# Performance work log

Hardware: AMD Instinct MI355X
Metric: run time of the kernel (lower is better)

Reference implementation:

```python
import jax, jax.numpy as jnp
import numpy as np

B, LH, HF = 65536, 128, 32
VC_MIN = 0.0


def _theta_init():
    # Deterministic parameter init, matching the torch constructor defaults.
    def spinv(x):
        return float(np.log(np.exp(max(x, 1e-4)) - 1.0 + 1e-6))
    vals = [
        0.0,                                  # alpha_raw: log(0.5/(1-0.5))
        float(np.log(np.exp(1.0) - 1.0 + 1e-6)),   # c_raw  (c_init=1.0)
        float(np.log(np.exp(0.1) - 1.0 + 1e-6)),   # kappa_raw (kappa_init=0.1)
        float(np.log(np.exp(0.15) - 1.0 + 1e-6)),  # vc_raw (vc_eff=0.15)
        -6.0,   # log_qx
        -6.0,   # log_qu
        -5.0,   # log_r
        0.0,    # log_q_scale
        -6.0,   # log_p0_xx
        -4.0,   # log_p0_uu
        spinv(0.1),   # a1_raw
        spinv(0.05),  # d1_raw
        spinv(0.5),   # d2_raw
        spinv(0.5),   # d3_raw
        0.0,    # b1
        0.0,    # b2
        0.1,    # beta
        float(np.arctanh(0.9)),  # rho_m_raw
        -4.0,   # log_qm
        -4.0,   # log_p0_mm
    ]
    return np.asarray(vals, dtype=np.float32)


def setup_inputs() -> dict:
    key = jax.random.key(0)
    k1, k2, k3, k4, k5 = jax.random.split(key, 5)
    return {
        "v_hist": jax.random.normal(k1, (B, LH), dtype=jnp.float32),
        "dt_hist": 0.01 + 0.1 * jax.random.uniform(k2, (B, LH), dtype=jnp.float32),
        "x_obs_hist": jax.random.normal(k3, (B, LH), dtype=jnp.float32),
        "v_fut": jax.random.normal(k4, (B, HF), dtype=jnp.float32),
        "dt_fut": 0.01 + 0.1 * jax.random.uniform(k5, (B, HF), dtype=jnp.float32),
        "theta": jnp.asarray(_theta_init()),
    }


def _forward(v_hist, dt_hist, x_obs_hist, v_fut, dt_fut, theta):
    sp = jax.nn.softplus
    alpha = jax.nn.sigmoid(theta[0])
    c = sp(theta[1]); kappa = sp(theta[2]); vc = sp(theta[3]) + VC_MIN
    qx = jnp.exp(theta[4]); qu = jnp.exp(theta[5]); R = jnp.exp(theta[6])
    qs = jnp.exp(theta[7]); p0xx = jnp.exp(theta[8]); p0uu = jnp.exp(theta[9])
    a1 = sp(theta[10]); d1 = sp(theta[11]); d2 = sp(theta[12]); d3 = sp(theta[13])
    b1 = theta[14]; b2 = theta[15]; beta = theta[16]
    rho_m = jnp.tanh(theta[17]); qm = jnp.exp(theta[18]); p0mm = jnp.exp(theta[19])

    Bn, Lh = v_hist.shape
    dtype = v_hist.dtype
    eye = jnp.eye(3, dtype=dtype)

    def predict(s, P, v, dv, dt):
        x, u, m = s[:, 0], s[:, 1], s[:, 2]
        rho = jnp.exp(-alpha * dt)
        forcing = jax.nn.relu(v * v - vc * vc)
        cl = (-a1 * u + b1 * v + b2 * dv
              - d1 * u * u - d2 * u * jnp.abs(v) - d3 * u * jnp.abs(u))
        x_p = x + u * dt
        u_p = rho * u - kappa * x * dt + c * forcing * dt + cl * dt + beta * m
        m_p = rho_m * m
        s_p = jnp.stack([x_p, u_p, m_p], axis=1)
        z = jnp.zeros_like(dt); o = jnp.ones_like(dt)
        Fm = jnp.stack([
            jnp.stack([o, dt, z], axis=1),
            jnp.stack([-kappa * dt, rho, beta * o], axis=1),
            jnp.stack([z, z, rho_m * o], axis=1)], axis=1)  # [B,3,3]
        qdiag = jnp.stack([qs * qx * dt, qs * qu * dt, qm * o], axis=1)  # [B,3]
        P_p = jnp.einsum('bij,bjk,blk->bil', Fm, P, Fm) + qdiag[:, :, None] * eye
        return s_p, P_p

    def update(s, P, y):
        innov = y - s[:, 0]
        S = P[:, 0, 0] + R
        K = P[:, :, 0] / S[:, None]            # [B,3]
        s_u = s + K * innov[:, None]
        IKH = eye - K[:, :, None] * eye[0]     # I - K H, H = [1,0,0]
        P_u = (jnp.einsum('bij,bjk,blk->bil', IKH, P, IKH)
               + R * (K[:, :, None] * K[:, None, :]))
        return s_u, P_u

    s0 = jnp.zeros((Bn, 3), dtype).at[:, 0].set(x_obs_hist[:, 0])
    P0 = jnp.broadcast_to(jnp.diag(jnp.stack([p0xx, p0uu, p0mm])).astype(dtype),
                          (Bn, 3, 3))

    # History steps k = 1 .. Lh-1 (scan over time axis, [T, B] layout)
    v_h = v_hist[:, :Lh - 1].T
    dv_h = jnp.concatenate(
        [jnp.zeros((1, Bn), dtype), (v_hist[:, 1:Lh - 1] - v_hist[:, :Lh - 2]).T], axis=0)
    dt_h = jnp.maximum(dt_hist[:, 1:], 1e-6).T
    y_h = x_obs_hist[:, 1:].T

    def hist_step(carry, inp):
        s, P = carry
        v, dv, dt, y = inp
        s, P = predict(s, P, v, dv, dt)
        s, P = update(s, P, y)
        return (s, P), None

    (s, P), _ = jax.lax.scan(hist_step, (s0, P0), (v_h, dv_h, dt_h, y_h))

    # Future rollout (predict only)
    v_f = v_fut.T
    dv_f = (v_fut - jnp.concatenate([v_hist[:, -1:], v_fut[:, :-1]], axis=1)).T
    dt_f = jnp.maximum(dt_fut, 1e-6).T

    def fut_step(carry, inp):
        s, P = carry
        v, dv, dt = inp
        s, P = predict(s, P, v, dv, dt)
        return (s, P), (s[:, 0], P[:, 0, 0], s[:, 1])

    _, (x_preds, x_vars, u_ests) = jax.lax.scan(fut_step, (s, P), (v_f, dv_f, dt_f))
    return x_preds.T, x_vars.T, u_ests.T  # each [B, Hf]


def reference(v_hist, dt_hist, x_obs_hist, v_fut, dt_fut, theta):
    return _forward(v_hist, dt_hist, x_obs_hist, v_fut, dt_fut, theta)
```

## Files before the change

kernel.cpp:

```cpp
#include <hip/hip_runtime.h>
#include <math.h>

#define BATCH 65536
#define LHIST 128
#define HFUT  32

__device__ __forceinline__ float softplusf(float x) {
    return fmaxf(x, 0.0f) + log1pf(expf(-fabsf(x)));
}

__global__ __launch_bounds__(256) void kalman_fwd(
    const float* __restrict__ v_hist,
    const float* __restrict__ dt_hist,
    const float* __restrict__ x_obs,
    const float* __restrict__ v_fut,
    const float* __restrict__ dt_fut,
    const float* __restrict__ theta,
    float* __restrict__ out)
{
    const int b = blockIdx.x * blockDim.x + threadIdx.x;

    const float alpha = 1.0f / (1.0f + expf(-theta[0]));
    const float c     = softplusf(theta[1]);
    const float kappa = softplusf(theta[2]);
    const float vc    = softplusf(theta[3]);
    const float qx    = expf(theta[4]);
    const float qu    = expf(theta[5]);
    const float Rn    = expf(theta[6]);
    const float qs    = expf(theta[7]);
    const float p0xx  = expf(theta[8]);
    const float p0uu  = expf(theta[9]);
    const float a1    = softplusf(theta[10]);
    const float d1    = softplusf(theta[11]);
    const float d2    = softplusf(theta[12]);
    const float d3    = softplusf(theta[13]);
    const float b1    = theta[14];
    const float b2    = theta[15];
    const float beta  = theta[16];
    const float rho_m = tanhf(theta[17]);
    const float qm    = expf(theta[18]);
    const float p0mm  = expf(theta[19]);
    const float vc2   = vc * vc;
    const float qxs   = qs * qx;
    const float qus   = qs * qu;

    float sx, su = 0.0f, sm = 0.0f;
    float p00 = p0xx, p01 = 0.0f, p02 = 0.0f, p11 = p0uu, p12 = 0.0f, p22 = p0mm;

    auto predict = [&](float v, float dv, float dt_raw) {
        float dt  = fmaxf(dt_raw, 1e-6f);
        float rho = expf(-alpha * dt);
        float forcing = fmaxf(v * v - vc2, 0.0f);
        float cl = -a1 * su + b1 * v + b2 * dv
                 - d1 * su * su - d2 * su * fabsf(v) - d3 * su * fabsf(su);
        float kdt = kappa * dt;
        float x_p = sx + su * dt;
        float u_p = rho * su - kdt * sx + c * forcing * dt + cl * dt + beta * sm;
        float m_p = rho_m * sm;
        float f0 = p00 + dt * p01;
        float f1 = p01 + dt * p11;
        float f2 = p02 + dt * p12;
        float g0 = -kdt * p00 + rho * p01 + beta * p02;
        float g1 = -kdt * p01 + rho * p11 + beta * p12;
        float g2 = -kdt * p02 + rho * p12 + beta * p22;
        float n00 = f0 + dt * f1 + qxs * dt;
        float n01 = -kdt * f0 + rho * f1 + beta * f2;
        float n02 = rho_m * f2;
        float n11 = -kdt * g0 + rho * g1 + beta * g2 + qus * dt;
        float n12 = rho_m * g2;
        float n22 = rho_m * rho_m * p22 + qm;
        sx = x_p; su = u_p; sm = m_p;
        p00 = n00; p01 = n01; p02 = n02; p11 = n11; p12 = n12; p22 = n22;
    };

    auto update = [&](float y) {
        float innov = y - sx;
        float S    = p00 + Rn;
        float Sinv = __builtin_amdgcn_rcpf(S);
        float K0 = p00 * Sinv, K1 = p01 * Sinv, K2 = p02 * Sinv;
        sx += K0 * innov; su += K1 * innov; sm += K2 * innov;
        float a = 1.0f - K0;
        float n00 = a * a * p00 + Rn * K0 * K0;
        float n01 = a * (p01 - K1 * p00) + Rn * K0 * K1;
        float n02 = a * (p02 - K2 * p00) + Rn * K0 * K2;
        float n11 = S * K1 * K1 - 2.0f * K1 * p01 + p11;
        float n12 = S * K1 * K2 - K2 * p01 - K1 * p02 + p12;
        float n22 = S * K2 * K2 - 2.0f * K2 * p02 + p22;
        p00 = n00; p01 = n01; p02 = n02; p11 = n11; p12 = n12; p22 = n22;
    };

    const float4* v4 = (const float4*)(v_hist  + (size_t)b * LHIST);
    const float4* d4 = (const float4*)(dt_hist + (size_t)b * LHIST);
    const float4* y4 = (const float4*)(x_obs   + (size_t)b * LHIST);

    float4 vq = v4[0], dq = d4[0], yq = y4[0];
    float4 vn = v4[1], dn = d4[1], yn = y4[1];
    sx = yq.x;

    predict(vq.x, 0.0f,        dq.y); update(yq.y);
    predict(vq.y, vq.y - vq.x, dq.z); update(yq.z);
    predict(vq.z, vq.z - vq.y, dq.w); update(yq.w);

    #pragma unroll 1
    for (int q = 1; q < 31; ++q) {
        float4 v2 = v4[q + 1], d2 = d4[q + 1], y2 = y4[q + 1];
        predict(vq.w, vq.w - vq.z, dn.x); update(yn.x);
        predict(vn.x, vn.x - vq.w, dn.y); update(yn.y);
        predict(vn.y, vn.y - vn.x, dn.z); update(yn.z);
        predict(vn.z, vn.z - vn.y, dn.w); update(yn.w);
        vq = vn; vn = v2; dn = d2; yn = y2;
    }
    predict(vq.w, vq.w - vq.z, dn.x); update(yn.x);
    predict(vn.x, vn.x - vq.w, dn.y); update(yn.y);
    predict(vn.y, vn.y - vn.x, dn.z); update(yn.z);
    predict(vn.z, vn.z - vn.y, dn.w); update(yn.w);
    float v_prev = vn.w;

    const float4* vf4 = (const float4*)(v_fut  + (size_t)b * HFUT);
    const float4* df4 = (const float4*)(dt_fut + (size_t)b * HFUT);
    float4* xp = (float4*)(out + (size_t)b * HFUT);
    float4* xv = (float4*)(out + (size_t)BATCH * HFUT + (size_t)b * HFUT);
    float4* ue = (float4*)(out + 2 * (size_t)BATCH * HFUT + (size_t)b * HFUT);

    #pragma unroll 1
    for (int q = 0; q < HFUT / 4; ++q) {
        float4 vf = vf4[q], df = df4[q];
        float4 oxp, oxv, oue;
        predict(vf.x, vf.x - v_prev, df.x); oxp.x = sx; oxv.x = p00; oue.x = su;
        predict(vf.y, vf.y - vf.x,   df.y); oxp.y = sx; oxv.y = p00; oue.y = su;
        predict(vf.z, vf.z - vf.y,   df.z); oxp.z = sx; oxv.z = p00; oue.z = su;
        predict(vf.w, vf.w - vf.z,   df.w); oxp.w = sx; oxv.w = p00; oue.w = su;
        v_prev = vf.w;
        xp[q] = oxp; xv[q] = oxv; ue[q] = oue;
    }
}

extern "C" void kernel_launch(void* const* d_in, const int* in_sizes, int n_in,
                              void* d_out, int out_size, void* d_ws, size_t ws_size,
                              hipStream_t stream) {
    const float* v_hist  = (const float*)d_in[0];
    const float* dt_hist = (const float*)d_in[1];
    const float* x_obs   = (const float*)d_in[2];
    const float* v_fut   = (const float*)d_in[3];
    const float* dt_fut  = (const float*)d_in[4];
    const float* theta   = (const float*)d_in[5];
    float* out = (float*)d_out;

    dim3 grid(BATCH / 256), block(256);
    hipLaunchKernelGGL(kalman_fwd, grid, block, 0, stream,
                       v_hist, dt_hist, x_obs, v_fut, dt_fut, theta, out);
}
```

Before: 199.0 us.

## Batch history loads in 32-step register chunks and prefetch future inputs

The history loop now loads 32 timesteps of v, dt and y into register arrays per chunk and fully unrolls the filter steps inside each chunk. Previously it prefetched only one float4 ahead. The future inputs are loaded up front, and all future outputs are buffered in registers and written at the end. Launch bounds are set to one block minimum, which allows many more registers. The aim is more memory-level parallelism and fewer load stalls, at the cost of much higher register pressure, lower occupancy and possible spills.

```diff
diff --git a/kernel.cpp b/kernel.cpp
--- a/kernel.cpp
+++ b/kernel.cpp
@@ -9,7 +9,7 @@
     return fmaxf(x, 0.0f) + log1pf(expf(-fabsf(x)));
 }
 
-__global__ __launch_bounds__(256) void kalman_fwd(
+__global__ __launch_bounds__(256, 1) void kalman_fwd(
     const float* __restrict__ v_hist,
     const float* __restrict__ dt_hist,
     const float* __restrict__ x_obs,
@@ -44,7 +44,7 @@
     const float qxs   = qs * qx;
     const float qus   = qs * qu;
 
-    float sx, su = 0.0f, sm = 0.0f;
+    float sx = 0.0f, su = 0.0f, sm = 0.0f;
     float p00 = p0xx, p01 = 0.0f, p02 = 0.0f, p11 = p0uu, p12 = 0.0f, p22 = p0mm;
 
     auto predict = [&](float v, float dv, float dt_raw) {
@@ -89,49 +89,62 @@
         p00 = n00; p01 = n01; p02 = n02; p11 = n11; p12 = n12; p22 = n22;
     };
 
-    const float4* v4 = (const float4*)(v_hist  + (size_t)b * LHIST);
-    const float4* d4 = (const float4*)(dt_hist + (size_t)b * LHIST);
-    const float4* y4 = (const float4*)(x_obs   + (size_t)b * LHIST);
+    const float4* v4  = (const float4*)(v_hist  + (size_t)b * LHIST);
+    const float4* d4  = (const float4*)(dt_hist + (size_t)b * LHIST);
+    const float4* y4  = (const float4*)(x_obs   + (size_t)b * LHIST);
+    const float4* vf4 = (const float4*)(v_fut   + (size_t)b * HFUT);
+    const float4* df4 = (const float4*)(dt_fut  + (size_t)b * HFUT);
 
-    float4 vq = v4[0], dq = d4[0], yq = y4[0];
-    float4 vn = v4[1], dn = d4[1], yn = y4[1];
-    sx = yq.x;
+    float vf[HFUT], df[HFUT];
+    {
+        float4* VF = (float4*)vf; float4* DF = (float4*)df;
+        #pragma unroll
+        for (int i = 0; i < HFUT / 4; ++i) { VF[i] = vf4[i]; DF[i] = df4[i]; }
+    }
 
-    predict(vq.x, 0.0f,        dq.y); update(yq.y);
-    predict(vq.y, vq.y - vq.x, dq.z); update(yq.z);
-    predict(vq.z, vq.z - vq.y, dq.w); update(yq.w);
+    float v_bridge = 0.0f, dv_bridge = 0.0f;
 
     #pragma unroll 1
-    for (int q = 1; q < 31; ++q) {
-        float4 v2 = v4[q + 1], d2 = d4[q + 1], y2 = y4[q + 1];
-        predict(vq.w, vq.w - vq.z, dn.x); update(yn.x);
-        predict(vn.x, vn.x - vq.w, dn.y); update(yn.y);
-        predict(vn.y, vn.y - vn.x, dn.z); update(yn.z);
-        predict(vn.z, vn.z - vn.y, dn.w); update(yn.w);
-        vq = vn; vn = v2; dn = d2; yn = y2;
+    for (int k = 0; k < 4; ++k) {
+        float vv[32], dd[32], yy[32];
+        float4* V = (float4*)vv; float4* D = (float4*)dd; float4* Y = (float4*)yy;
+        #pragma unroll
+        for (int i = 0; i < 8; ++i) {
+            V[i] = v4[8 * k + i];
+            D[i] = d4[8 * k + i];
+            Y[i] = y4[8 * k + i];
+        }
+        if (k == 0) {
+            sx = yy[0];
+            predict(vv[0], 0.0f, dd[1]); update(yy[1]);
+        } else {
+            predict(v_bridge, dv_bridge, dd[0]); update(yy[0]);
+            predict(vv[0], vv[0] - v_bridge, dd[1]); update(yy[1]);
+        }
+        #pragma unroll
+        for (int i = 1; i < 31; ++i) {
+            predict(vv[i], vv[i] - vv[i - 1], dd[i + 1]); update(yy[i + 1]);
+        }
+        v_bridge  = vv[31];
+        dv_bridge = vv[31] - vv[30];
     }
-    predict(vq.w, vq.w - vq.z, dn.x); update(yn.x);
-    predict(vn.x, vn.x - vq.w, dn.y); update(yn.y);
-    predict(vn.y, vn.y - vn.x, dn.z); update(yn.z);
-    predict(vn.z, vn.z - vn.y, dn.w); update(yn.w);
-    float v_prev = vn.w;
 
-    const float4* vf4 = (const float4*)(v_fut  + (size_t)b * HFUT);
-    const float4* df4 = (const float4*)(dt_fut + (size_t)b * HFUT);
+    float oxp[HFUT], oxv[HFUT], oue[HFUT];
+    float vp = v_bridge;
+    #pragma unroll
+    for (int j = 0; j < HFUT; ++j) {
+        predict(vf[j], vf[j] - vp, df[j]);
+        vp = vf[j];
+        oxp[j] = sx; oxv[j] = p00; oue[j] = su;
+    }
+
     float4* xp = (float4*)(out + (size_t)b * HFUT);
     float4* xv = (float4*)(out + (size_t)BATCH * HFUT + (size_t)b * HFUT);
     float4* ue = (float4*)(out + 2 * (size_t)BATCH * HFUT + (size_t)b * HFUT);
-
-    #pragma unroll 1
-    for (int q = 0; q < HFUT / 4; ++q) {
-        float4 vf = vf4[q], df = df4[q];
-        float4 oxp, oxv, oue;
-        predict(vf.x, vf.x - v_prev, df.x); oxp.x = sx; oxv.x = p00; oue.x = su;
-        predict(vf.y, vf.y - vf.x,   df.y); oxp.y = sx; oxv.y = p00; oue.y = su;
-        predict(vf.z, vf.z - vf.y,   df.z); oxp.z = sx; oxv.z = p00; oue.z = su;
-        predict(vf.w, vf.w - vf.z,   df.w); oxp.w = sx; oxv.w = p00; oue.w = su;
-        v_prev = vf.w;
-        xp[q] = oxp; xv[q] = oxv; ue[q] = oue;
+    float4* OXP = (float4*)oxp; float4* OXV = (float4*)oxv; float4* OUE = (float4*)oue;
+    #pragma unroll
+    for (int i = 0; i < HFUT / 4; ++i) {
+        xp[i] = OXP[i]; xv[i] = OXV[i]; ue[i] = OUE[i];
     }
 }
 
```

Result: faster. 186.9 us (-6.1%).

## Double-buffer 16-step history chunks and batch future loads and stores

Applied to the files above, without the earlier changes.

Restructures the history loop into 16-step chunks held in two register buffers (A/B), so each chunk's loads are issued one chunk ahead of its compute. The future rollout now loads all inputs up front, before the last history chunk, and defers every output store to the end. It also swaps expf for a hardware exp2 with a prescaled constant and sets launch bounds to (256,1). The cost being targeted is memory latency per thread. The price is much higher register pressure, which can lower occupancy and reduce latency hiding across waves.

```diff
diff --git a/kernel.cpp b/kernel.cpp
--- a/kernel.cpp
+++ b/kernel.cpp
@@ -9,7 +9,7 @@
     return fmaxf(x, 0.0f) + log1pf(expf(-fabsf(x)));
 }
 
-__global__ __launch_bounds__(256) void kalman_fwd(
+__global__ __launch_bounds__(256, 1) void kalman_fwd(
     const float* __restrict__ v_hist,
     const float* __restrict__ dt_hist,
     const float* __restrict__ x_obs,
@@ -18,7 +18,7 @@
     const float* __restrict__ theta,
     float* __restrict__ out)
 {
-    const int b = blockIdx.x * blockDim.x + threadIdx.x;
+    const int b = blockIdx.x * 256 + threadIdx.x;
 
     const float alpha = 1.0f / (1.0f + expf(-theta[0]));
     const float c     = softplusf(theta[1]);
@@ -43,13 +43,14 @@
     const float vc2   = vc * vc;
     const float qxs   = qs * qx;
     const float qus   = qs * qu;
-
-    float sx, su = 0.0f, sm = 0.0f;
+    const float nal2e = -alpha * 1.44269504088896340736f;
+
+    float sx = 0.0f, su = 0.0f, sm = 0.0f;
     float p00 = p0xx, p01 = 0.0f, p02 = 0.0f, p11 = p0uu, p12 = 0.0f, p22 = p0mm;
 
     auto predict = [&](float v, float dv, float dt_raw) {
         float dt  = fmaxf(dt_raw, 1e-6f);
-        float rho = expf(-alpha * dt);
+        float rho = __builtin_amdgcn_exp2f(nal2e * dt);
         float forcing = fmaxf(v * v - vc2, 0.0f);
         float cl = -a1 * su + b1 * v + b2 * dv
                  - d1 * su * su - d2 * su * fabsf(v) - d3 * su * fabsf(su);
@@ -93,46 +94,100 @@
     const float4* d4 = (const float4*)(dt_hist + (size_t)b * LHIST);
     const float4* y4 = (const float4*)(x_obs   + (size_t)b * LHIST);
 
-    float4 vq = v4[0], dq = d4[0], yq = y4[0];
-    float4 vn = v4[1], dn = d4[1], yn = y4[1];
-    sx = yq.x;
-
-    predict(vq.x, 0.0f,        dq.y); update(yq.y);
-    predict(vq.y, vq.y - vq.x, dq.z); update(yq.z);
-    predict(vq.z, vq.z - vq.y, dq.w); update(yq.w);
+    float4 AV0, AV1, AV2, AV3, AD0, AD1, AD2, AD3, AY0, AY1, AY2, AY3;
+    float4 BV0, BV1, BV2, BV3, BD0, BD1, BD2, BD3, BY0, BY1, BY2, BY3;
+    float vp1 = 0.0f, vp2 = 0.0f;
+
+#define LOAD_CHUNK(k, P) do {                                                    \
+    P##V0 = v4[4*(k)+0]; P##V1 = v4[4*(k)+1];                                    \
+    P##V2 = v4[4*(k)+2]; P##V3 = v4[4*(k)+3];                                    \
+    P##D0 = d4[4*(k)+0]; P##D1 = d4[4*(k)+1];                                    \
+    P##D2 = d4[4*(k)+2]; P##D3 = d4[4*(k)+3];                                    \
+    P##Y0 = y4[4*(k)+0]; P##Y1 = y4[4*(k)+1];                                    \
+    P##Y2 = y4[4*(k)+2]; P##Y3 = y4[4*(k)+3];                                    \
+} while (0)
+
+#define KSTEP(vc_, vpv_, dtn_, yn_) do { predict((vc_), (vc_) - (vpv_), (dtn_)); update(yn_); } while (0)
+
+#define CHUNK_TAIL(P) do {                                                       \
+    KSTEP(P##V0.y, P##V0.x, P##D0.z, P##Y0.z);                                   \
+    KSTEP(P##V0.z, P##V0.y, P##D0.w, P##Y0.w);                                   \
+    KSTEP(P##V0.w, P##V0.z, P##D1.x, P##Y1.x);                                   \
+    KSTEP(P##V1.x, P##V0.w, P##D1.y, P##Y1.y);                                   \
+    KSTEP(P##V1.y, P##V1.x, P##D1.z, P##Y1.z);                                   \
+    KSTEP(P##V1.z, P##V1.y, P##D1.w, P##Y1.w);                                   \
+    KSTEP(P##V1.w, P##V1.z, P##D2.x, P##Y2.x);                                   \
+    KSTEP(P##V2.x, P##V1.w, P##D2.y, P##Y2.y);                                   \
+    KSTEP(P##V2.y, P##V2.x, P##D2.z, P##Y2.z);                                   \
+    KSTEP(P##V2.z, P##V2.y, P##D2.w, P##Y2.w);                                   \
+    KSTEP(P##V2.w, P##V2.z, P##D3.x, P##Y3.x);                                   \
+    KSTEP(P##V3.x, P##V2.w, P##D3.y, P##Y3.y);                                   \
+    KSTEP(P##V3.y, P##V3.x, P##D3.z, P##Y3.z);                                   \
+    KSTEP(P##V3.z, P##V3.y, P##D3.w, P##Y3.w);                                   \
+    vp2 = P##V3.z; vp1 = P##V3.w;                                                \
+} while (0)
+
+#define CHUNK(P) do {                                                            \
+    predict(vp1, vp1 - vp2, P##D0.x);   update(P##Y0.x);                         \
+    KSTEP(P##V0.x, vp1, P##D0.y, P##Y0.y);                                       \
+    CHUNK_TAIL(P);                                                               \
+} while (0)
+
+    LOAD_CHUNK(0, A);
+    LOAD_CHUNK(1, B);
+
+    sx = AY0.x;
+    predict(AV0.x, 0.0f, AD0.y); update(AY0.y);
+    CHUNK_TAIL(A);
 
     #pragma unroll 1
-    for (int q = 1; q < 31; ++q) {
-        float4 v2 = v4[q + 1], d2 = d4[q + 1], y2 = y4[q + 1];
-        predict(vq.w, vq.w - vq.z, dn.x); update(yn.x);
-        predict(vn.x, vn.x - vq.w, dn.y); update(yn.y);
-        predict(vn.y, vn.y - vn.x, dn.z); update(yn.z);
-        predict(vn.z, vn.z - vn.y, dn.w); update(yn.w);
-        vq = vn; vn = v2; dn = d2; yn = y2;
+    for (int k = 1; k <= 3; ++k) {
+        LOAD_CHUNK(2 * k, A);
+        CHUNK(B);
+        LOAD_CHUNK(2 * k + 1, B);
+        CHUNK(A);
     }
-    predict(vq.w, vq.w - vq.z, dn.x); update(yn.x);
-    predict(vn.x, vn.x - vq.w, dn.y); update(yn.y);
-    predict(vn.y, vn.y - vn.x, dn.z); update(yn.z);
-    predict(vn.z, vn.z - vn.y, dn.w); update(yn.w);
-    float v_prev = vn.w;
 
     const float4* vf4 = (const float4*)(v_fut  + (size_t)b * HFUT);
     const float4* df4 = (const float4*)(dt_fut + (size_t)b * HFUT);
+    float4 VF0 = vf4[0], VF1 = vf4[1], VF2 = vf4[2], VF3 = vf4[3],
+           VF4 = vf4[4], VF5 = vf4[5], VF6 = vf4[6], VF7 = vf4[7];
+    float4 DF0 = df4[0], DF1 = df4[1], DF2 = df4[2], DF3 = df4[3],
+           DF4 = df4[4], DF5 = df4[5], DF6 = df4[6], DF7 = df4[7];
+
+    CHUNK(B);
+
+    float4 OP0, OP1, OP2, OP3, OP4, OP5, OP6, OP7;
+    float4 OV0, OV1, OV2, OV3, OV4, OV5, OV6, OV7;
+    float4 OU0, OU1, OU2, OU3, OU4, OU5, OU6, OU7;
+    float vp = vp1;
+
+#define FUTQ(VF, DF, OP, OV, OU) do {                                            \
+    predict(VF.x, VF.x - vp,   DF.x); OP.x = sx; OV.x = p00; OU.x = su;          \
+    predict(VF.y, VF.y - VF.x, DF.y); OP.y = sx; OV.y = p00; OU.y = su;          \
+    predict(VF.z, VF.z - VF.y, DF.z); OP.z = sx; OV.z = p00; OU.z = su;          \
+    predict(VF.w, VF.w - VF.z, DF.w); OP.w = sx; OV.w = p00; OU.w = su;          \
+    vp = VF.w;                                                                   \
+} while (0)
+
+    FUTQ(VF0, DF0, OP0, OV0, OU0);
+    FUTQ(VF1, DF1, OP1, OV1, OU1);
+    FUTQ(VF2, DF2, OP2, OV2, OU2);
+    FUTQ(VF3, DF3, OP3, OV3, OU3);
+    FUTQ(VF4, DF4, OP4, OV4, OU4);
+    FUTQ(VF5, DF5, OP5, OV5, OU5);
+    FUTQ(VF6, DF6, OP6, OV6, OU6);
+    FUTQ(VF7, DF7, OP7, OV7, OU7);
+
     float4* xp = (float4*)(out + (size_t)b * HFUT);
     float4* xv = (float4*)(out + (size_t)BATCH * HFUT + (size_t)b * HFUT);
     float4* ue = (float4*)(out + 2 * (size_t)BATCH * HFUT + (size_t)b * HFUT);
-
-    #pragma unroll 1
-    for (int q = 0; q < HFUT / 4; ++q) {
-        float4 vf = vf4[q], df = df4[q];
-        float4 oxp, oxv, oue;
-        predict(vf.x, vf.x - v_prev, df.x); oxp.x = sx; oxv.x = p00; oue.x = su;
-        predict(vf.y, vf.y - vf.x,   df.y); oxp.y = sx; oxv.y = p00; oue.y = su;
-        predict(vf.z, vf.z - vf.y,   df.z); oxp.z = sx; oxv.z = p00; oue.z = su;
-        predict(vf.w, vf.w - vf.z,   df.w); oxp.w = sx; oxv.w = p00; oue.w = su;
-        v_prev = vf.w;
-        xp[q] = oxp; xv[q] = oxv; ue[q] = oue;
-    }
+    xp[0] = OP0; xp[1] = OP1; xp[2] = OP2; xp[3] = OP3;
+    xp[4] = OP4; xp[5] = OP5; xp[6] = OP6; xp[7] = OP7;
+    xv[0] = OV0; xv[1] = OV1; xv[2] = OV2; xv[3] = OV3;
+    xv[4] = OV4; xv[5] = OV5; xv[6] = OV6; xv[7] = OV7;
+    ue[0] = OU0; ue[1] = OU1; ue[2] = OU2; ue[3] = OU3;
+    ue[4] = OU4; ue[5] = OU5; ue[6] = OU6; ue[7] = OU7;
 }
 
 extern "C" void kernel_launch(void* const* d_in, const int* in_sizes, int n_in,
```

Measured after the change: 167.6 us. 15.8% less time.
